# Kernel tuning notes

Measured on AMD Instinct MI355X. Metric: run time of the kernel, lower is better.

Reference implementation:

```python
import jax, jax.numpy as jnp
import numpy as np

B, T, C, H = 4, 2048, 768, 12
D = C // H  # head_dim = 64
ROPE_BASE = 10000.0


def _make_rope_cache(seq_len, n_elem, base=ROPE_BASE):
    theta = 1.0 / base ** (jnp.arange(0, n_elem, 2, dtype=jnp.float32) / n_elem)  # [D/2]
    idx_theta = jnp.arange(seq_len, dtype=jnp.float32)[:, None] * theta[None, :]  # [T, D/2]
    return jnp.stack([jnp.cos(idx_theta), jnp.sin(idx_theta)], axis=-1)  # [T, D/2, 2]


def setup_inputs() -> dict:
    key = jax.random.key(0)
    k1, k2, k3 = jax.random.split(key, 3)
    x = jax.random.normal(k1, (B, T, C), dtype=jnp.float32)
    rope_cache = _make_rope_cache(T, D)
    w_qkv = jax.random.normal(k2, (3 * C, C), dtype=jnp.float32) * (1.0 / np.sqrt(C))
    w_o = jax.random.normal(k3, (C, C), dtype=jnp.float32) * (1.0 / np.sqrt(C))
    return {"x": x, "rope_cache": rope_cache, "w_qkv": w_qkv, "w_o": w_o}


def _apply_rope(t, cos, sin):
    # t: [B,T,H,D]; cos/sin: [T,D/2] broadcast to [1,T,1,D/2]
    tp = t.reshape(t.shape[:-1] + (D // 2, 2))
    t0, t1 = tp[..., 0], tp[..., 1]
    c = cos[None, :, None, :]
    s = sin[None, :, None, :]
    rot = jnp.stack([t0 * c - t1 * s, t0 * s + t1 * c], axis=-1)
    return rot.reshape(t.shape)


def reference(x, rope_cache, w_qkv, w_o):
    b, t, c = x.shape
    qkv = (x @ w_qkv.T).reshape(b, t, 3, H, D)
    q, k, v = qkv[:, :, 0], qkv[:, :, 1], qkv[:, :, 2]  # [B,T,H,D]
    cos = rope_cache[:t, :, 0]
    sin = rope_cache[:t, :, 1]
    q = _apply_rope(q, cos, sin)
    k = _apply_rope(k, cos, sin)
    scale = 1.0 / np.sqrt(D)
    att = jnp.einsum('bqhd,bkhd->bhqk', q, k) * scale  # [B,H,T,T]
    causal = jnp.tril(jnp.ones((t, t), dtype=bool))
    att = jnp.where(causal[None, None], att, jnp.finfo(att.dtype).min)
    att = jax.nn.softmax(att, axis=-1)
    y = jnp.einsum('bhqk,bkhd->bqhd', att, v).reshape(b, t, c)
    return y @ w_o.T
```

## Files before the change

kernel.cpp:

```cpp
#include <hip/hip_runtime.h>

#define B_  4
#define T_  2048
#define C_  768
#define H_  12
#define D_  64

typedef unsigned short u16;
typedef unsigned int   u32;
typedef __bf16 bf16;
typedef __bf16 bf16x4 __attribute__((ext_vector_type(4)));
typedef __bf16 bf16x8 __attribute__((ext_vector_type(8)));
typedef float  f32x4  __attribute__((ext_vector_type(4)));
typedef float  f32x16 __attribute__((ext_vector_type(16)));
typedef u32    u32x4  __attribute__((ext_vector_type(4)));
typedef __attribute__((address_space(1))) void* gas_t;
typedef __attribute__((address_space(3))) void* las_t;

static __device__ __forceinline__ u16 f2bf(float f) {
  u32 u = __builtin_bit_cast(u32, f);
  u += 0x7FFFu + ((u >> 16) & 1u);
  return (u16)(u >> 16);
}

static __device__ __forceinline__ u32 cvtpk(float a, float b) {
  u32 r;
  asm("v_cvt_pk_bf16_f32 %0, %1, %2" : "=v"(r) : "v"(a), "v"(b));
  return r;
}
static __device__ __forceinline__ void plswap(u32& a, u32& b) {
  asm volatile("v_permlane32_swap_b32 %0, %1" : "+v"(a), "+v"(b));
}

__global__ __launch_bounds__(256) void k_cvt3(const float* __restrict__ a0,
                                              const float* __restrict__ a1,
                                              const float* __restrict__ a2,
                                              u16* __restrict__ o0,
                                              u16* __restrict__ o1,
                                              u16* __restrict__ o2) {
  const int bid = blockIdx.x;
  const int tid = threadIdx.x;
  if (bid < 6144) {
    const int i = bid * 256 + tid;
    const float4 v = ((const float4*)a0)[i];
    ushort4 o;
    o.x = f2bf(v.x); o.y = f2bf(v.y); o.z = f2bf(v.z); o.w = f2bf(v.w);
    ((ushort4*)o0)[i] = o;
  } else if (bid < 7872) {
    const int i = (bid - 6144) * 256 + tid;
    const int n = i / 192;
    const int c4 = i - n * 192;
    int n2 = n;
    if (n < 1536) {
      const int d = n & 63;
      const int c = (((d & 1) | ((d >> 5) << 1)) << 4) | ((d >> 1) & 15);
      n2 = (n & ~63) | c;
    }
    const float4 v = ((const float4*)a1)[i];
    ushort4 o;
    o.x = f2bf(v.x); o.y = f2bf(v.y); o.z = f2bf(v.z); o.w = f2bf(v.w);
    ((ushort4*)o1)[n2 * 192 + c4] = o;
  } else {
    const int i = (bid - 7872) * 256 + tid;
    const float4 v = ((const float4*)a2)[i];
    ushort4 o;
    o.x = f2bf(v.x); o.y = f2bf(v.y); o.z = f2bf(v.z); o.w = f2bf(v.w);
    ((ushort4*)o2)[i] = o;
  }
}

template<int MODE, int BM>
__global__ __launch_bounds__(256) void k_gemm_bt(const u16* __restrict__ A,
                                                 const u16* __restrict__ Bt,
                                                 float* __restrict__ Cout,
                                                 u16* __restrict__ qout,
                                                 u16* __restrict__ kout,
                                                 u16* __restrict__ vout,
                                                 const float* __restrict__ rope,
                                                 int M, int N, int K) {
  constexpr int NJ = (BM == 128) ? 4 : 2;
  constexpr int PA = BM / 32;
  constexpr int NB = (BM == 64) ? 2 : 1;
  __shared__ u16 lA[NB * BM * 64];
  __shared__ u16 lB[NB * 128 * 64];
  const int tid = threadIdx.x;
  const int l = tid & 63, w = tid >> 6;
  const int lo = l & 15, hi = l >> 4;
  const int wrow = (BM == 128) ? (w >> 1) * 64 : 0;
  const int wcol = (BM == 128) ? (w & 1) * 64 : w * 32;
  const int pid = blockIdx.x + gridDim.x * blockIdx.y;
  const int total = gridDim.x * gridDim.y;
  const int lid = (pid & 7) * (total >> 3) + (pid >> 3);
  const int bx = lid % gridDim.x, by = lid / gridDim.x;
  const int m0 = by * BM, n0 = bx * 128;

  const int srow_t = tid >> 3;
  const int scb   = ((tid & 7) * 16) ^ ((srow_t & 7) << 4);
  const int swz   = (lo & 7) << 4;

  auto STAGE = [&](int bufi, int k0) {
#pragma unroll
    for (int p = 0; p < PA; ++p)
      __builtin_amdgcn_global_load_lds(
          (gas_t)(u16*)(A + (size_t)(m0 + srow_t + 32 * p) * K + k0 + (scb >> 1)),
          (las_t)(lA + bufi * BM * 64 + p * 2048 + tid * 8), 16, 0, 0);
#pragma unroll
    for (int p = 0; p < 4; ++p)
      __builtin_amdgcn_global_load_lds(
          (gas_t)(u16*)(Bt + (size_t)(n0 + srow_t + 32 * p) * K + k0 + (scb >> 1)),
          (las_t)(lB + bufi * 128 * 64 + p * 2048 + tid * 8), 16, 0, 0);
  };

  f32x4 acc[4][NJ] = {};
  auto COMPUTE = [&](const u16* la, const u16* lb) {
#pragma unroll
    for (int kk = 0; kk < 2; ++kk) {
      const int co = ((kk * 64 + hi * 16) ^ swz) >> 1;
      bf16x8 af[4], bfr[NJ];
#pragma unroll
      for (int i = 0; i < 4; ++i)
        af[i] = *(const bf16x8*)(la + (wrow + i * 16 + lo) * 64 + co);
#pragma unroll
      for (int j = 0; j < NJ; ++j)
        bfr[j] = *(const bf16x8*)(lb + (wcol + j * 16 + lo) * 64 + co);
      __builtin_amdgcn_s_setprio(1);
#pragma unroll
      for (int i = 0; i < 4; ++i)
#pragma unroll
        for (int j = 0; j < NJ; ++j)
          acc[i][j] = __builtin_amdgcn_mfma_f32_16x16x32_bf16(af[i], bfr[j], acc[i][j], 0, 0, 0);
      __builtin_amdgcn_s_setprio(0);
    }
  };

  if (BM == 128) {
    for (int k0 = 0; k0 < K; k0 += 64) {
      STAGE(0, k0);
      asm volatile("s_waitcnt vmcnt(0)" ::: "memory");
      __builtin_amdgcn_s_barrier();
      __builtin_amdgcn_sched_barrier(0);
      COMPUTE(lA, lB);
      asm volatile("" ::: "memory");
      __builtin_amdgcn_s_barrier();
      __builtin_amdgcn_sched_barrier(0);
    }
  } else {
    STAGE(0, 0);
    asm volatile("s_waitcnt vmcnt(0)" ::: "memory");
    __builtin_amdgcn_s_barrier();
    __builtin_amdgcn_sched_barrier(0);
    int cur = 0;
    const int nk = K >> 6;
    for (int ks = 0; ks < nk; ++ks) {
      if (ks + 1 < nk) {
        STAGE(cur ^ 1, (ks + 1) * 64);
        asm volatile("s_waitcnt vmcnt(6)" ::: "memory");
      } else {
        asm volatile("s_waitcnt vmcnt(0)" ::: "memory");
      }
      __builtin_amdgcn_s_barrier();
      __builtin_amdgcn_sched_barrier(0);
      COMPUTE(lA + cur * BM * 64, lB + cur * 128 * 64);
      asm volatile("" ::: "memory");
      __builtin_amdgcn_s_barrier();
      __builtin_amdgcn_sched_barrier(0);
      cur ^= 1;
    }
  }

  const int crow = m0 + wrow;
  if (MODE == 1) {
#pragma unroll
    for (int i = 0; i < 4; ++i)
#pragma unroll
      for (int j = 0; j < NJ; ++j)
#pragma unroll
        for (int r = 0; r < 4; ++r)
          Cout[(size_t)(crow + i * 16 + hi * 4 + r) * N + n0 + wcol + j * 16 + lo] = acc[i][j][r];
  } else {
    const int wc = w & 1;
    const int sect = bx / 6;
    const int h2 = (bx % 6) * 2 + wc;
    if (sect < 2) {
      const float qsc = (sect == 0) ? 0.18033688011f : 1.0f;
      u16* dst = (sect == 0) ? qout : kout;
#pragma unroll
      for (int i = 0; i < 4; ++i)
#pragma unroll
        for (int r = 0; r < 4; ++r) {
          const int trow = crow + i * 16 + hi * 4 + r;
          const int t = trow & (T_ - 1), bb = trow >> 11;
          const float2 cs0 = *(const float2*)(rope + ((size_t)t * 32 + lo) * 2);
          const float2 cs1 = *(const float2*)(rope + ((size_t)t * 32 + 16 + lo) * 2);
          const float a0 = acc[i][0][r], a1 = acc[i][1][r];
          const float a2 = acc[i][2][r], a3 = acc[i][3][r];
          const float e0 = (a0 * cs0.x - a1 * cs0.y) * qsc;
          const float e1 = (a0 * cs0.y + a1 * cs0.x) * qsc;
          const float e2 = (a2 * cs1.x - a3 * cs1.y) * qsc;
          const float e3 = (a2 * cs1.y + a3 * cs1.x) * qsc;
          u16* row = dst + ((size_t)(bb * H_ + h2) * T_ + t) * D_;
          *(ushort2*)(row + 2 * lo)      = make_ushort2(f2bf(e0), f2bf(e1));
          *(ushort2*)(row + 32 + 2 * lo) = make_ushort2(f2bf(e2), f2bf(e3));
        }
    } else {
#pragma unroll
      for (int i = 0; i < 4; ++i)
#pragma unroll
        for (int j = 0; j < NJ; ++j)
#pragma unroll
          for (int r = 0; r < 4; ++r) {
            const int trow = crow + i * 16 + hi * 4 + r;
            vout[(size_t)trow * C_ + h2 * D_ + j * 16 + lo] = f2bf(acc[i][j][r]);
          }
    }
  }
}

__global__ __launch_bounds__(256) void k_vtrans(const u16* __restrict__ vtmp,
                                                u16* __restrict__ vt) {
  __shared__ u16 lds[64][68];
  const int bid = blockIdx.x;
  const int ttile = bid & 31, bh = bid >> 5;
  const int b = bh / H_, h = bh % H_;
  const int tid = threadIdx.x;
  const int tl = tid >> 2, doff = (tid & 3) * 16;
  const u16* src = vtmp + (size_t)(b * T_ + ttile * 64 + tl) * C_ + h * D_ + doff;
  const uint4 v0 = *(const uint4*)(src);
  const uint4 v1 = *(const uint4*)(src + 8);
  *(uint2*)&lds[tl][doff + 0]  = make_uint2(v0.x, v0.y);
  *(uint2*)&lds[tl][doff + 4]  = make_uint2(v0.z, v0.w);
  *(uint2*)&lds[tl][doff + 8]  = make_uint2(v1.x, v1.y);
  *(uint2*)&lds[tl][doff + 12] = make_uint2(v1.z, v1.w);
  __syncthreads();
  const int d = tl, toff = doff;
  uint4 o0, o1;
#define PK(j) ((u32)lds[toff + (j)][d] | ((u32)lds[toff + (j) + 1][d] << 16))
  o0.x = PK(0);  o0.y = PK(2);  o0.z = PK(4);  o0.w = PK(6);
  o1.x = PK(8);  o1.y = PK(10); o1.z = PK(12); o1.w = PK(14);
#undef PK
  u16* dst = vt + ((size_t)bh * D_ + d) * T_ + ttile * 64 + toff;
  *(uint4*)(dst) = o0;
  *(uint4*)(dst + 8) = o1;
}

__global__ __launch_bounds__(256) void k_attn(const u16* __restrict__ qb,
                                              const u16* __restrict__ kb,
                                              const u16* __restrict__ vtb,
                                              u16* __restrict__ yb) {
  __shared__ u16 kbuf[2][64 * 64];
  __shared__ u16 vbuf[2][64 * 64];
  __shared__ float obuf[2][64][33];
  __shared__ float lbuf[2][64];
  const int tid = threadIdx.x;
  const int w = tid >> 6, l = tid & 63;
  const int q5 = l & 31, hf = l >> 5;
  const int qg = w >> 1, st = w & 1;
  const int pid = blockIdx.x;
  const int xcd = pid & 7;
  const int rank = pid >> 3;
  const int p = rank / 6;
  const int bh = xcd * 6 + rank % 6;
  const int h = bh % H_, b = bh / H_;
  const u16* Q  = qb  + (size_t)bh * T_ * D_;
  const u16* K  = kb  + (size_t)bh * T_ * D_;
  const u16* Vt = vtb + (size_t)bh * D_ * T_;
  const int segA = 16 + p, segB = 15 - p;
  const int ntA = segA + 1;

  const int srow = tid >> 3;
  const int scb  = ((tid & 7) * 16) ^ ((srow & 7) << 4);
  const int swz  = (l & 7) << 4;

#define STAGE(bufi, j0s)                                                             \
  do {                                                                               \
    __builtin_amdgcn_global_load_lds((gas_t)(u16*)(K + (size_t)((j0s) + srow) * D_ + (scb >> 1)),      \
                                     (las_t)(&kbuf[bufi][0] + tid * 8), 16, 0, 0);   \
    __builtin_amdgcn_global_load_lds((gas_t)(u16*)(K + (size_t)((j0s) + 32 + srow) * D_ + (scb >> 1)), \
                                     (las_t)(&kbuf[bufi][0] + (tid + 256) * 8), 16, 0, 0);             \
    __builtin_amdgcn_global_load_lds((gas_t)(u16*)(Vt + (size_t)srow * T_ + (j0s) + (scb >> 1)),       \
                                     (las_t)(&vbuf[bufi][0] + tid * 8), 16, 0, 0);   \
    __builtin_amdgcn_global_load_lds((gas_t)(u16*)(Vt + (size_t)(32 + srow) * T_ + (j0s) + (scb >> 1)),\
                                     (las_t)(&vbuf[bufi][0] + (tid + 256) * 8), 16, 0, 0);             \
  } while (0)

  int seg = segA;
  int q0w = seg * 64 + qg * 32;
  int q = q0w + q5;
  bf16x8 qf[4];
#pragma unroll
  for (int dc = 0; dc < 4; ++dc)
    qf[dc] = *(const bf16x8*)(Q + (size_t)q * D_ + dc * 16 + hf * 8);

  const f32x16 Z = {};
  f32x16 o0 = {}, o1 = {};
  float ls0 = 0.f, ls1 = 0.f, ls2 = 0.f, ls3 = 0.f;

  STAGE(0, 0);
  int cur = 0;
  for (int flat = 0; flat < 33; ++flat) {
    const int local = (flat < ntA) ? flat : flat - ntA;
    const int j0 = local * 64;
    asm volatile("s_waitcnt vmcnt(0)" ::: "memory");
    __builtin_amdgcn_s_barrier();
    __builtin_amdgcn_sched_barrier(0);
    if (flat + 1 < 33) {
      const int nloc = (flat + 1 < ntA) ? flat + 1 : flat + 1 - ntA;
      STAGE(cur ^ 1, nloc * 64);
    }
    if (j0 + 32 * st <= q0w + 31) {
      const u16* kb_l = &kbuf[cur][0];
      const u16* vb_l = &vbuf[cur][0];
      f32x16 s;
      __builtin_amdgcn_s_setprio(1);
      {
        const int krow = st * 32 + q5;
        const bf16x8 kd0 = *(const bf16x8*)(kb_l + krow * 64 + (((0  + 16 * hf) ^ swz) >> 1));
        s = __builtin_amdgcn_mfma_f32_32x32x16_bf16(kd0, qf[0], Z, 0, 0, 0);
        const bf16x8 kd1 = *(const bf16x8*)(kb_l + krow * 64 + (((32 + 16 * hf) ^ swz) >> 1));
        s = __builtin_amdgcn_mfma_f32_32x32x16_bf16(kd1, qf[1], s, 0, 0, 0);
        const bf16x8 kd2 = *(const bf16x8*)(kb_l + krow * 64 + (((64 + 16 * hf) ^ swz) >> 1));
        s = __builtin_amdgcn_mfma_f32_32x32x16_bf16(kd2, qf[2], s, 0, 0, 0);
        const bf16x8 kd3 = *(const bf16x8*)(kb_l + krow * 64 + (((96 + 16 * hf) ^ swz) >> 1));
        s = __builtin_amdgcn_mfma_f32_32x32x16_bf16(kd3, qf[3], s, 0, 0, 0);
      }
      __builtin_amdgcn_s_setprio(0);
      if (local == seg) {
#pragma unroll
        for (int r = 0; r < 16; ++r) {
          const int kv = j0 + 32 * st + (r & 3) + 8 * (r >> 2) + 4 * hf;
          if (kv > q) s[r] = -1e30f;
        }
      }
#pragma unroll
      for (int r = 0; r < 16; ++r)
        s[r] = __builtin_amdgcn_exp2f(s[r]);
#pragma unroll
      for (int r = 0; r < 16; r += 4) {
        ls0 += s[r]; ls1 += s[r + 1]; ls2 += s[r + 2]; ls3 += s[r + 3];
      }
      u32 a0 = cvtpk(s[0],  s[1]),  b0 = cvtpk(s[4],  s[5]);  plswap(a0, b0);
      u32 a1 = cvtpk(s[2],  s[3]),  b1 = cvtpk(s[6],  s[7]);  plswap(a1, b1);
      u32 a2 = cvtpk(s[8],  s[9]),  b2 = cvtpk(s[12], s[13]); plswap(a2, b2);
      u32 a3 = cvtpk(s[10], s[11]), b3 = cvtpk(s[14], s[15]); plswap(a3, b3);
      const bf16x8 pa0 = __builtin_bit_cast(bf16x8, (u32x4){a0, a1, b0, b1});
      const bf16x8 pa1 = __builtin_bit_cast(bf16x8, (u32x4){a2, a3, b2, b3});
      __builtin_amdgcn_s_setprio(1);
      {
        const int ks0 = st * 2, ks1 = st * 2 + 1;
        const bf16x8 vf00 = *(const bf16x8*)(vb_l + q5 * 64        + (((ks0 * 32 + 16 * hf) ^ swz) >> 1));
        const bf16x8 vf10 = *(const bf16x8*)(vb_l + (32 + q5) * 64 + (((ks0 * 32 + 16 * hf) ^ swz) >> 1));
        o0 = __builtin_amdgcn_mfma_f32_32x32x16_bf16(vf00, pa0, o0, 0, 0, 0);
        o1 = __builtin_amdgcn_mfma_f32_32x32x16_bf16(vf10, pa0, o1, 0, 0, 0);
        const bf16x8 vf01 = *(const bf16x8*)(vb_l + q5 * 64        + (((ks1 * 32 + 16 * hf) ^ swz) >> 1));
        const bf16x8 vf11 = *(const bf16x8*)(vb_l + (32 + q5) * 64 + (((ks1 * 32 + 16 * hf) ^ swz) >> 1));
        o0 = __builtin_amdgcn_mfma_f32_32x32x16_bf16(vf01, pa1, o0, 0, 0, 0);
        o1 = __builtin_amdgcn_mfma_f32_32x32x16_bf16(vf11, pa1, o1, 0, 0, 0);
      }
      __builtin_amdgcn_s_setprio(0);
    }
    if (local == seg) {
      if (st == 1) {
        float* ob = &obuf[qg][l][0];
#pragma unroll
        for (int r = 0; r < 16; ++r) { ob[r] = o0[r]; ob[16 + r] = o1[r]; }
        float lr = (ls0 + ls1) + (ls2 + ls3);
        lr += __shfl_xor(lr, 32);
        lbuf[qg][l] = lr;
        asm volatile("s_waitcnt lgkmcnt(0)" ::: "memory");
      }
      asm volatile("" ::: "memory");
      __builtin_amdgcn_s_barrier();
      __builtin_amdgcn_sched_barrier(0);
      if (st == 0) {
        const float* ob = &obuf[qg][l][0];
#pragma unroll
        for (int r = 0; r < 16; ++r) { o0[r] += ob[r]; o1[r] += ob[16 + r]; }
        float lr = (ls0 + ls1) + (ls2 + ls3);
        lr += __shfl_xor(lr, 32);
        const float lt = lr + lbuf[qg][l];
        const float linv = 1.0f / lt;
        u16* yrow = yb + (size_t)(b * T_ + q) * C_ + h * D_;
#pragma unroll
        for (int g = 0; g < 4; ++g) {
          bf16x4 ok0, ok1;
#pragma unroll
          for (int r = 0; r < 4; ++r) {
            ok0[r] = (__bf16)(o0[4 * g + r] * linv);
            ok1[r] = (__bf16)(o1[4 * g + r] * linv);
          }
          *(bf16x4*)(yrow + g * 8 + 4 * hf)      = ok0;
          *(bf16x4*)(yrow + 32 + g * 8 + 4 * hf) = ok1;
        }
      }
      if (flat < 32) {
        seg = segB;
        q0w = seg * 64 + qg * 32;
        q = q0w + q5;
#pragma unroll
        for (int dc = 0; dc < 4; ++dc)
          qf[dc] = *(const bf16x8*)(Q + (size_t)q * D_ + dc * 16 + hf * 8);
      }
      o0 = Z; o1 = Z;
      ls0 = 0.f; ls1 = 0.f; ls2 = 0.f; ls3 = 0.f;
    }
    cur ^= 1;
  }
#undef STAGE
}

extern "C" void kernel_launch(void* const* d_in, const int* in_sizes, int n_in,
                              void* d_out, int out_size, void* d_ws, size_t ws_size,
                              hipStream_t stream) {
  (void)in_sizes; (void)n_in; (void)out_size; (void)ws_size;
  const float* x    = (const float*)d_in[0];
  const float* rope = (const float*)d_in[1];
  const float* wqkv = (const float*)d_in[2];
  const float* wo   = (const float*)d_in[3];
  float* out = (float*)d_out;
  char* ws = (char*)d_ws;
  u16* xb    = (u16*)(ws);
  u16* wqkvb = (u16*)(ws + 12582912);
  u16* wob   = (u16*)(ws + 16121856);
  u16* vtmp  = (u16*)(ws + 17301504);
  u16* qb    = (u16*)(ws + 55050240);
  u16* kb    = (u16*)(ws + 67633152);
  u16* vtb   = (u16*)(ws + 80216064);
  u16* yb    = xb;

  k_cvt3<<<8448, 256, 0, stream>>>(x, wqkv, wo, xb, wqkvb, wob);
  k_gemm_bt<2, 128><<<dim3(18, 64), 256, 0, stream>>>(xb, wqkvb, nullptr, qb, kb, vtmp,
                                                      rope, 8192, 2304, 768);
  k_vtrans<<<1536, 256, 0, stream>>>(vtmp, vtb);
  k_attn<<<768, 256, 0, stream>>>(qb, kb, vtb, yb);
  k_gemm_bt<1, 64><<<dim3(6, 128), 256, 0, stream>>>(yb, wob, out, nullptr, nullptr, nullptr,
                                                     nullptr, 8192, 768, 768);
}
```

Measured before the change: 118.6 us.

## Double-buffer LDS for all GEMM tile sizes with one barrier per k-step

The BM=128 GEMM path previously used a single LDS buffer, staging and computing serially with two barriers per k-step. Now both tile sizes use a double-buffered loop: the next tile is staged into the alternate buffer while the current one is computed, with one wait-and-barrier per iteration. This aims to overlap global-to-LDS loads with MFMA work and cut barrier overhead. It doubles LDS use for BM=128, which may lower occupancy. The single barrier placed before staging may also leave a race with warps still reading the buffer being overwritten.

```diff
diff --git a/kernel.cpp b/kernel.cpp
--- a/kernel.cpp
+++ b/kernel.cpp
@@ -80,9 +80,8 @@
                                                  int M, int N, int K) {
   constexpr int NJ = (BM == 128) ? 4 : 2;
   constexpr int PA = BM / 32;
-  constexpr int NB = (BM == 64) ? 2 : 1;
-  __shared__ u16 lA[NB * BM * 64];
-  __shared__ u16 lB[NB * 128 * 64];
+  __shared__ u16 lA[2 * BM * 64];
+  __shared__ u16 lB[2 * 128 * 64];
   const int tid = threadIdx.x;
   const int l = tid & 63, w = tid >> 6;
   const int lo = l & 15, hi = l >> 4;
@@ -133,39 +132,16 @@
     }
   };
 
-  if (BM == 128) {
-    for (int k0 = 0; k0 < K; k0 += 64) {
-      STAGE(0, k0);
-      asm volatile("s_waitcnt vmcnt(0)" ::: "memory");
-      __builtin_amdgcn_s_barrier();
-      __builtin_amdgcn_sched_barrier(0);
-      COMPUTE(lA, lB);
-      asm volatile("" ::: "memory");
-      __builtin_amdgcn_s_barrier();
-      __builtin_amdgcn_sched_barrier(0);
-    }
-  } else {
-    STAGE(0, 0);
+  STAGE(0, 0);
+  int cur = 0;
+  const int nk = K >> 6;
+  for (int ks = 0; ks < nk; ++ks) {
     asm volatile("s_waitcnt vmcnt(0)" ::: "memory");
     __builtin_amdgcn_s_barrier();
     __builtin_amdgcn_sched_barrier(0);
-    int cur = 0;
-    const int nk = K >> 6;
-    for (int ks = 0; ks < nk; ++ks) {
-      if (ks + 1 < nk) {
-        STAGE(cur ^ 1, (ks + 1) * 64);
-        asm volatile("s_waitcnt vmcnt(6)" ::: "memory");
-      } else {
-        asm volatile("s_waitcnt vmcnt(0)" ::: "memory");
-      }
-      __builtin_amdgcn_s_barrier();
-      __builtin_amdgcn_sched_barrier(0);
-      COMPUTE(lA + cur * BM * 64, lB + cur * 128 * 64);
-      asm volatile("" ::: "memory");
-      __builtin_amdgcn_s_barrier();
-      __builtin_amdgcn_sched_barrier(0);
-      cur ^= 1;
-    }
+    if (ks + 1 < nk) STAGE(cur ^ 1, (ks + 1) * 64);
+    COMPUTE(lA + cur * BM * 64, lB + cur * 128 * 64);
+    cur ^= 1;
   }
 
   const int crow = m0 + wrow;
```

New measurement: 125.8 us. +6.0%, slower.
